# Kernel optimization log

Hardware: AMD Instinct MI355X
Metric: run time of the kernel (lower is better)

Reference implementation:

```python
import jax, jax.numpy as jnp
import numpy as np

DIM = 768
NUM_HEADS = 8
GROUPS = 2


def setup_inputs() -> dict:
    key = jax.random.key(0)
    ks = jax.random.split(key, 6)
    B, N, C = 8, 1024, DIM
    x = jax.random.normal(ks[0], (B, N, C), dtype=jnp.float32)
    # nn.Linear weights stored (out_features, in_features), applied as x @ W.T
    w_qkv = jax.random.normal(ks[1], (3 * C, C), dtype=jnp.float32) * 0.02
    g_dim = C // GROUPS
    w_g0 = jax.random.normal(ks[2], (3 * g_dim, g_dim), dtype=jnp.float32) * 0.02
    w_g1 = jax.random.normal(ks[3], (3 * g_dim, g_dim), dtype=jnp.float32) * 0.02
    w_proj = jax.random.normal(ks[4], (C, C), dtype=jnp.float32) * 0.02
    b_proj = jax.random.normal(ks[5], (C,), dtype=jnp.float32) * 0.02
    return {"x": x, "w_qkv": w_qkv, "w_g0": w_g0, "w_g1": w_g1,
            "w_proj": w_proj, "b_proj": b_proj}


def reference(x, w_qkv, w_g0, w_g1, w_proj, b_proj):
    B, N, C = x.shape
    H = NUM_HEADS
    hd = C // H
    scale = hd ** (-0.5)  # qk_scale=None -> head_dim^-0.5, reused in group attn
    g = GROUPS
    g_dim = C // g

    # ---- standard MHSA branch ----
    qkv = (x @ w_qkv.T).reshape(B, N, 3, H, hd)
    qkv = jnp.transpose(qkv, (2, 0, 3, 1, 4))  # (3, B, H, N, hd)
    q, k, v = qkv[0], qkv[1], qkv[2]
    attn = jax.nn.softmax(jnp.einsum('bhnd,bhmd->bhnm', q, k) * scale, axis=-1)
    origin = jnp.einsum('bhnm,bhmd->bhnd', attn, v)  # (B, H, N, hd)
    origin = origin.swapaxes(1, 2).reshape(B, N, g, g_dim)

    # ---- sequential per-group head-fusion branch ----
    xg = x.reshape(B, N, g, g_dim)
    head_x = jnp.zeros((B, N, g_dim), dtype=x.dtype)
    outputs = []
    for i, w in enumerate([w_g0, w_g1]):  # fixed small loop, g=2
        cur = xg[:, :, i] + head_x
        qkv2 = (cur @ w.T).reshape(B, N, 3, g_dim)
        q2, k2, v2 = qkv2[:, :, 0], qkv2[:, :, 1], qkv2[:, :, 2]
        a2 = jax.nn.softmax(jnp.einsum('bnd,bmd->bnm', q2, k2) * scale, axis=-1)
        head_x = jnp.einsum('bnm,bmd->bnd', a2, v2)
        outputs.append(head_x + origin[:, :, i])

    out = jnp.concatenate(outputs, axis=-1)
    return out @ w_proj.T + b_proj
```

## Files before the change

### kernel.cpp

```cpp
#include <hip/hip_runtime.h>
#include <cstdint>
#include <cstddef>

#define DEV_INLINE __device__ __forceinline__

typedef __bf16 bf16;
typedef __bf16 bf16x8 __attribute__((ext_vector_type(8)));
typedef float f32x4 __attribute__((ext_vector_type(4)));

static constexpr int Bb = 8;
static constexpr int Nn = 1024;
static constexpr int Cc = 768;
static constexpr int HD = 96;
static constexpr int GD = 384;
#define SCALE_ 0.1020620726159658f

DEV_INLINE void gload_lds16(void* lds, const void* g) {
  __builtin_amdgcn_global_load_lds(
      (__attribute__((address_space(1))) void*)(void*)g,
      (__attribute__((address_space(3))) void*)lds, 16, 0, 0);
}

__global__ void k_f32_to_bf16(const float* __restrict__ src, bf16* __restrict__ dst, int n) {
  int i = (blockIdx.x * 256 + threadIdx.x) * 8;
  if (i >= n) return;
  float4 a = *(const float4*)(src + i);
  float4 b = *(const float4*)(src + i + 4);
  bf16x8 o;
  o[0] = (bf16)a.x; o[1] = (bf16)a.y; o[2] = (bf16)a.z; o[3] = (bf16)a.w;
  o[4] = (bf16)b.x; o[5] = (bf16)b.y; o[6] = (bf16)b.z; o[7] = (bf16)b.w;
  *(bf16x8*)(dst + i) = o;
}

__global__ void k_make_cur(const float* __restrict__ x, const float* __restrict__ hx,
                           bf16* __restrict__ cur, int gi) {
  int t = blockIdx.x * 256 + threadIdx.x;
  int m = t / 48;
  int d0 = (t % 48) * 8;
  const float* xr = x + (size_t)m * Cc + gi * GD + d0;
  float4 a = *(const float4*)xr;
  float4 b = *(const float4*)(xr + 4);
  if (gi) {
    const float* hr = hx + (size_t)m * GD + d0;
    float4 c = *(const float4*)hr;
    float4 d = *(const float4*)(hr + 4);
    a.x += c.x; a.y += c.y; a.z += c.z; a.w += c.w;
    b.x += d.x; b.y += d.y; b.z += d.z; b.w += d.w;
  }
  bf16x8 o;
  o[0] = (bf16)a.x; o[1] = (bf16)a.y; o[2] = (bf16)a.z; o[3] = (bf16)a.w;
  o[4] = (bf16)b.x; o[5] = (bf16)b.y; o[6] = (bf16)b.z; o[7] = (bf16)b.w;
  *(bf16x8*)(cur + (size_t)m * GD + d0) = o;
}

template <int EPI>
__global__ __launch_bounds__(256, 2)
void k_gemm(const bf16* __restrict__ A, const bf16* __restrict__ W, int K,
            int aZ, int wZ,
            bf16* __restrict__ o0, bf16* __restrict__ o1, bf16* __restrict__ o2,
            float* __restrict__ f0, const float* __restrict__ bias,
            const float* __restrict__ origin, int gi) {
  const int bm = blockIdx.x, bn = blockIdx.y, bz = blockIdx.z;
  const int tid = threadIdx.x;
  const int wave = tid >> 6, lane = tid & 63;
  const int wr = wave >> 1, wc = wave & 1;
  const int l15 = lane & 15, l4 = lane >> 4;

  A += (size_t)bz * aZ;
  W += (size_t)bz * wZ;

  __shared__ bf16 As[128 * 32];
  __shared__ bf16 Bs[128 * 32];

  f32x4 acc[4][4] = {};

  const int t8 = tid * 8;
  const int r0 = t8 >> 5, c0 = t8 & 31;
  const int r1 = r0 + 64;
  const bf16* Arow0 = A + (size_t)(bm * 128 + r0) * K + c0;
  const bf16* Arow1 = A + (size_t)(bm * 128 + r1) * K + c0;
  const bf16* Brow0 = W + (size_t)(bn * 128 + r0) * K + c0;
  const bf16* Brow1 = W + (size_t)(bn * 128 + r1) * K + c0;
  bf16* sA0 = &As[wave * 512];
  bf16* sA1 = &As[2048 + wave * 512];
  bf16* sB0 = &Bs[wave * 512];
  bf16* sB1 = &Bs[2048 + wave * 512];

  for (int k0 = 0; k0 < K; k0 += 32) {
    gload_lds16(sA0, Arow0 + k0);
    gload_lds16(sA1, Arow1 + k0);
    gload_lds16(sB0, Brow0 + k0);
    gload_lds16(sB1, Brow1 + k0);
    __syncthreads();
    bf16x8 af[4], bfr[4];
#pragma unroll
    for (int i = 0; i < 4; ++i) {
      af[i]  = *(const bf16x8*)&As[(wr * 64 + i * 16 + l15) * 32 + l4 * 8];
      bfr[i] = *(const bf16x8*)&Bs[(wc * 64 + i * 16 + l15) * 32 + l4 * 8];
    }
#pragma unroll
    for (int i = 0; i < 4; ++i)
#pragma unroll
      for (int j = 0; j < 4; ++j)
        acc[i][j] = __builtin_amdgcn_mfma_f32_16x16x32_bf16(af[i], bfr[j], acc[i][j], 0, 0, 0);
    __syncthreads();
  }

#pragma unroll
  for (int i = 0; i < 4; ++i) {
    const int mbase = bm * 128 + wr * 64 + i * 16 + l4 * 4;
#pragma unroll
    for (int j = 0; j < 4; ++j) {
      const int col = bn * 128 + wc * 64 + j * 16 + l15;
#pragma unroll
      for (int r = 0; r < 4; ++r) {
        const int row = mbase + r;
        const float val = acc[i][j][r];
        if constexpr (EPI == 2) {
          f0[(size_t)row * 768 + col] = val + bias[col];
        } else if constexpr (EPI == 3) {
          o0[((size_t)bz * 1024 + row) * 1024 + col] = (bf16)(val * SCALE_);
        } else if constexpr (EPI == 4) {
          const size_t gr = (size_t)bz * 1024 + row;
          f0[gr * 384 + col] = val;
          const size_t ci = gr * 768 + gi * 384 + col;
          o1[ci] = (bf16)(val + origin[ci]);
        } else if constexpr (EPI == 0) {
          const int bb = row >> 10, n = row & 1023;
          const int sct = col / 768, rem = col % 768;
          const int hh = rem / 96, dd = rem % 96;
          const bf16 bv = (bf16)val;
          if (sct == 0)      o0[((size_t)(bb * 8 + hh) * 1024 + n) * 96 + dd] = bv;
          else if (sct == 1) o1[((size_t)(bb * 8 + hh) * 1024 + n) * 96 + dd] = bv;
          else               o2[((size_t)(bb * 8 + hh) * 96 + dd) * 1024 + n] = bv;
        } else {
          const int bb = row >> 10, n = row & 1023;
          const int sct = col / 384, dd = col % 384;
          const bf16 bv = (bf16)val;
          if (sct == 0)      o0[(size_t)row * 384 + dd] = bv;
          else if (sct == 1) o1[(size_t)row * 384 + dd] = bv;
          else               o2[((size_t)bb * 384 + dd) * 1024 + n] = bv;
        }
      }
    }
  }
}

__global__ __launch_bounds__(256)
void k_softmax_rows(bf16* __restrict__ SP) {
  const int row = blockIdx.x * 4 + (threadIdx.x >> 6);
  const int lane = threadIdx.x & 63;
  bf16* R = SP + (size_t)row * 1024 + lane * 16;
  bf16x8 a = *(const bf16x8*)R;
  bf16x8 b = *(const bf16x8*)(R + 8);
  float v[16];
#pragma unroll
  for (int i = 0; i < 8; ++i) { v[i] = (float)a[i]; v[8 + i] = (float)b[i]; }
  float mx = -1e30f;
#pragma unroll
  for (int i = 0; i < 16; ++i) mx = fmaxf(mx, v[i]);
  mx = fmaxf(mx, __shfl_xor(mx, 1));
  mx = fmaxf(mx, __shfl_xor(mx, 2));
  mx = fmaxf(mx, __shfl_xor(mx, 4));
  mx = fmaxf(mx, __shfl_xor(mx, 8));
  mx = fmaxf(mx, __shfl_xor(mx, 16));
  mx = fmaxf(mx, __shfl_xor(mx, 32));
  float s = 0.f;
#pragma unroll
  for (int i = 0; i < 16; ++i) { v[i] = __expf(v[i] - mx); s += v[i]; }
  s += __shfl_xor(s, 1);
  s += __shfl_xor(s, 2);
  s += __shfl_xor(s, 4);
  s += __shfl_xor(s, 8);
  s += __shfl_xor(s, 16);
  s += __shfl_xor(s, 32);
  const float inv = 1.f / s;
#pragma unroll
  for (int i = 0; i < 8; ++i) { a[i] = (bf16)(v[i] * inv); b[i] = (bf16)(v[8 + i] * inv); }
  *(bf16x8*)R = a;
  *(bf16x8*)(R + 8) = b;
}

__global__ __launch_bounds__(256, 2)
void k_flash_mha(const bf16* __restrict__ Q, const bf16* __restrict__ Kt,
                 const bf16* __restrict__ Vt, float* __restrict__ origin) {
  const int bh = blockIdx.x, qb = blockIdx.y;
  const int b = bh >> 3, h = bh & 7;
  const int wave = threadIdx.x >> 6, lane = threadIdx.x & 63;
  const int l15 = lane & 15, l4 = lane >> 4;
  const bf16* Qh = Q + (size_t)bh * Nn * HD;
  const bf16* Kh = Kt + (size_t)bh * Nn * HD;
  const bf16* Vh = Vt + (size_t)bh * HD * Nn;
  const int q0 = qb * 128 + wave * 32;

  bf16x8 qf[2][3];
#pragma unroll
  for (int mf = 0; mf < 2; ++mf)
#pragma unroll
    for (int kf = 0; kf < 3; ++kf)
      qf[mf][kf] = *(const bf16x8*)&Qh[(size_t)(q0 + mf * 16 + l15) * HD + kf * 32 + l4 * 8];

  f32x4 o[2][6] = {};
  float mrow[2][4], lrow[2][4];
#pragma unroll
  for (int mf = 0; mf < 2; ++mf)
#pragma unroll
    for (int r = 0; r < 4; ++r) { mrow[mf][r] = -1e30f; lrow[mf][r] = 0.f; }

  __shared__ bf16 Plds[4][32 * 88];
  bf16* Pl = &Plds[wave][0];

  for (int n0 = 0; n0 < Nn; n0 += 64) {
    f32x4 s[2][4] = {};
#pragma unroll
    for (int nf = 0; nf < 4; ++nf)
#pragma unroll
      for (int kf = 0; kf < 3; ++kf) {
        bf16x8 kfr = *(const bf16x8*)&Kh[(size_t)(n0 + nf * 16 + l15) * HD + kf * 32 + l4 * 8];
#pragma unroll
        for (int mf = 0; mf < 2; ++mf)
          s[mf][nf] = __builtin_amdgcn_mfma_f32_16x16x32_bf16(qf[mf][kf], kfr, s[mf][nf], 0, 0, 0);
      }
#pragma unroll
    for (int mf = 0; mf < 2; ++mf)
#pragma unroll
      for (int r = 0; r < 4; ++r) {
        float mx = -1e30f;
#pragma unroll
        for (int nf = 0; nf < 4; ++nf) {
          s[mf][nf][r] *= SCALE_;
          mx = fmaxf(mx, s[mf][nf][r]);
        }
        mx = fmaxf(mx, __shfl_xor(mx, 1));
        mx = fmaxf(mx, __shfl_xor(mx, 2));
        mx = fmaxf(mx, __shfl_xor(mx, 4));
        mx = fmaxf(mx, __shfl_xor(mx, 8));
        float mnew = fmaxf(mrow[mf][r], mx);
        float alpha = __expf(mrow[mf][r] - mnew);
        mrow[mf][r] = mnew;
        float ls = 0.f;
#pragma unroll
        for (int nf = 0; nf < 4; ++nf) {
          float p = __expf(s[mf][nf][r] - mnew);
          s[mf][nf][r] = p;
          ls += p;
        }
        ls += __shfl_xor(ls, 1); ls += __shfl_xor(ls, 2);
        ls += __shfl_xor(ls, 4); ls += __shfl_xor(ls, 8);
        lrow[mf][r] = lrow[mf][r] * alpha + ls;
#pragma unroll
        for (int df = 0; df < 6; ++df) o[mf][df][r] *= alpha;
      }
#pragma unroll
    for (int mf = 0; mf < 2; ++mf)
#pragma unroll
      for (int nf = 0; nf < 4; ++nf)
#pragma unroll
        for (int r = 0; r < 4; ++r)
          Pl[(mf * 16 + l4 * 4 + r) * 88 + nf * 16 + l15] = (bf16)s[mf][nf][r];
    bf16x8 pa[2][2];
#pragma unroll
    for (int mf = 0; mf < 2; ++mf)
#pragma unroll
      for (int kf2 = 0; kf2 < 2; ++kf2)
        pa[mf][kf2] = *(const bf16x8*)&Pl[(mf * 16 + l15) * 88 + kf2 * 32 + l4 * 8];
#pragma unroll
    for (int df = 0; df < 6; ++df)
#pragma unroll
      for (int kf2 = 0; kf2 < 2; ++kf2) {
        bf16x8 vf = *(const bf16x8*)&Vh[(size_t)(df * 16 + l15) * Nn + n0 + kf2 * 32 + l4 * 8];
#pragma unroll
        for (int mf = 0; mf < 2; ++mf)
          o[mf][df] = __builtin_amdgcn_mfma_f32_16x16x32_bf16(pa[mf][kf2], vf, o[mf][df], 0, 0, 0);
      }
  }

  float* Og = origin + (size_t)b * Nn * Cc + h * HD;
#pragma unroll
  for (int mf = 0; mf < 2; ++mf)
#pragma unroll
    for (int r = 0; r < 4; ++r) {
      const int row = q0 + mf * 16 + l4 * 4 + r;
      const float inv = 1.f / lrow[mf][r];
#pragma unroll
      for (int df = 0; df < 6; ++df)
        Og[(size_t)row * Cc + df * 16 + l15] = o[mf][df][r] * inv;
    }
}

extern "C" void kernel_launch(void* const* d_in, const int* in_sizes, int n_in,
                              void* d_out, int out_size, void* d_ws, size_t ws_size,
                              hipStream_t stream) {
  const float* x      = (const float*)d_in[0];
  const float* w_qkv  = (const float*)d_in[1];
  const float* w_g0   = (const float*)d_in[2];
  const float* w_g1   = (const float*)d_in[3];
  const float* w_proj = (const float*)d_in[4];
  const float* b_proj = (const float*)d_in[5];
  float* out = (float*)d_out;

  char* ws = (char*)d_ws;
  size_t off = 0;
  auto alloc = [&](size_t bytes) {
    char* p = ws + off;
    off += (bytes + 255) & ~(size_t)255;
    return p;
  };
  bf16* xb     = (bf16*)alloc((size_t)8192 * 768 * 2);
  bf16* wqkvb  = (bf16*)alloc((size_t)2304 * 768 * 2);
  bf16* wg0b   = (bf16*)alloc((size_t)1152 * 384 * 2);
  bf16* wg1b   = (bf16*)alloc((size_t)1152 * 384 * 2);
  bf16* wprojb = (bf16*)alloc((size_t)768 * 768 * 2);
  float* origin = (float*)alloc((size_t)8192 * 768 * 4);
  char* R = alloc((size_t)67108864);
  bf16* Qb = (bf16*)R;
  bf16* Kb = (bf16*)(R + 12582912);
  bf16* Vt = (bf16*)(R + 25165824);
  bf16* curb = (bf16*)R;
  bf16* q2   = (bf16*)(R + 6291456);
  bf16* k2   = (bf16*)(R + 12582912);
  bf16* v2t  = (bf16*)(R + 18874368);
  float* hx  = (float*)(R + 25165824);
  bf16* cat  = (bf16*)(R + 37748736);
  bf16* SP   = (bf16*)(R + 50331648);

  k_f32_to_bf16<<<dim3(3072), 256, 0, stream>>>(x, xb, 8192 * 768);
  k_f32_to_bf16<<<dim3(864), 256, 0, stream>>>(w_qkv, wqkvb, 2304 * 768);
  k_f32_to_bf16<<<dim3(216), 256, 0, stream>>>(w_g0, wg0b, 1152 * 384);
  k_f32_to_bf16<<<dim3(216), 256, 0, stream>>>(w_g1, wg1b, 1152 * 384);
  k_f32_to_bf16<<<dim3(288), 256, 0, stream>>>(w_proj, wprojb, 768 * 768);

  k_gemm<0><<<dim3(64, 18), 256, 0, stream>>>(xb, wqkvb, 768, 0, 0, Qb, Kb, Vt, nullptr, nullptr, nullptr, 0);
  k_flash_mha<<<dim3(64, 8), 256, 0, stream>>>(Qb, Kb, Vt, origin);

  for (int gi = 0; gi < 2; ++gi) {
    const bf16* wg = gi ? wg1b : wg0b;
    k_make_cur<<<dim3(1536), 256, 0, stream>>>(x, hx, curb, gi);
    k_gemm<1><<<dim3(64, 9), 256, 0, stream>>>(curb, wg, 384, 0, 0, q2, k2, v2t, nullptr, nullptr, nullptr, 0);
    k_gemm<3><<<dim3(8, 8, 8), 256, 0, stream>>>(q2, k2, 384, 1024 * 384, 1024 * 384,
                                                 SP, nullptr, nullptr, nullptr, nullptr, nullptr, 0);
    k_softmax_rows<<<dim3(2048), 256, 0, stream>>>(SP);
    k_gemm<4><<<dim3(8, 3, 8), 256, 0, stream>>>(SP, v2t, 1024, 1024 * 1024, 384 * 1024,
                                                 nullptr, cat, nullptr, hx, nullptr, origin, gi);
  }

  k_gemm<2><<<dim3(64, 6), 256, 0, stream>>>(cat, wprojb, 768, 0, 0, nullptr, nullptr, nullptr, out, b_proj, nullptr, 0);
}
```

Before: 448.8 us.

## Fuse input conversions, shrink flash tiles, add lazy softmax rescaling

Five f32-to-bf16 conversion launches are merged into one kernel that picks its source and destination by index range, removing launch overhead. The flash MHA kernel now gives each wave 16 query rows instead of 32, doubling the grid and raising launch bounds to 4 blocks per SM for more occupancy. Online softmax rescaling is skipped unless some row's running max grows by more than 8, cutting exp and multiply work. The trade-off is that K and V fragments are reused across fewer query rows, so global loads per MFMA double.

Result: no change. 453.5 us (+1.1%).

```diff
diff --git a/kernel.cpp b/kernel.cpp
--- a/kernel.cpp
+++ b/kernel.cpp
@@ -21,15 +21,25 @@
       (__attribute__((address_space(3))) void*)lds, 16, 0, 0);
 }
 
-__global__ void k_f32_to_bf16(const float* __restrict__ src, bf16* __restrict__ dst, int n) {
-  int i = (blockIdx.x * 256 + threadIdx.x) * 8;
-  if (i >= n) return;
-  float4 a = *(const float4*)(src + i);
-  float4 b = *(const float4*)(src + i + 4);
+__global__ void k_convert_all(const float* __restrict__ x, const float* __restrict__ wqkv,
+                              const float* __restrict__ wg0, const float* __restrict__ wg1,
+                              const float* __restrict__ wproj,
+                              bf16* __restrict__ xb, bf16* __restrict__ wqkvb,
+                              bf16* __restrict__ wg0b, bf16* __restrict__ wg1b,
+                              bf16* __restrict__ wprojb) {
+  const int i = (blockIdx.x * 256 + threadIdx.x) * 8;
+  const float* src; bf16* dst; int off;
+  if (i < 6291456)      { src = x;     dst = xb;     off = i; }
+  else if (i < 8060928) { src = wqkv;  dst = wqkvb;  off = i - 6291456; }
+  else if (i < 8503296) { src = wg0;   dst = wg0b;   off = i - 8060928; }
+  else if (i < 8945664) { src = wg1;   dst = wg1b;   off = i - 8503296; }
+  else                  { src = wproj; dst = wprojb; off = i - 8945664; }
+  float4 a = *(const float4*)(src + off);
+  float4 b = *(const float4*)(src + off + 4);
   bf16x8 o;
   o[0] = (bf16)a.x; o[1] = (bf16)a.y; o[2] = (bf16)a.z; o[3] = (bf16)a.w;
   o[4] = (bf16)b.x; o[5] = (bf16)b.y; o[6] = (bf16)b.z; o[7] = (bf16)b.w;
-  *(bf16x8*)(dst + i) = o;
+  *(bf16x8*)(dst + off) = o;
 }
 
 __global__ void k_make_cur(const float* __restrict__ x, const float* __restrict__ hx,
@@ -181,7 +191,7 @@
   *(bf16x8*)(R + 8) = b;
 }
 
-__global__ __launch_bounds__(256, 2)
+__global__ __launch_bounds__(256, 4)
 void k_flash_mha(const bf16* __restrict__ Q, const bf16* __restrict__ Kt,
                  const bf16* __restrict__ Vt, float* __restrict__ origin) {
   const int bh = blockIdx.x, qb = blockIdx.y;
@@ -191,101 +201,99 @@
   const bf16* Qh = Q + (size_t)bh * Nn * HD;
   const bf16* Kh = Kt + (size_t)bh * Nn * HD;
   const bf16* Vh = Vt + (size_t)bh * HD * Nn;
-  const int q0 = qb * 128 + wave * 32;
-
-  bf16x8 qf[2][3];
-#pragma unroll
-  for (int mf = 0; mf < 2; ++mf)
-#pragma unroll
-    for (int kf = 0; kf < 3; ++kf)
-      qf[mf][kf] = *(const bf16x8*)&Qh[(size_t)(q0 + mf * 16 + l15) * HD + kf * 32 + l4 * 8];
-
-  f32x4 o[2][6] = {};
-  float mrow[2][4], lrow[2][4];
-#pragma unroll
-  for (int mf = 0; mf < 2; ++mf)
-#pragma unroll
-    for (int r = 0; r < 4; ++r) { mrow[mf][r] = -1e30f; lrow[mf][r] = 0.f; }
-
-  __shared__ bf16 Plds[4][32 * 88];
+  const int q0 = qb * 64 + wave * 16;
+
+  bf16x8 qf[3];
+#pragma unroll
+  for (int kf = 0; kf < 3; ++kf)
+    qf[kf] = *(const bf16x8*)&Qh[(size_t)(q0 + l15) * HD + kf * 32 + l4 * 8];
+
+  f32x4 o[6] = {};
+  float mrow[4], lrow[4];
+#pragma unroll
+  for (int r = 0; r < 4; ++r) { mrow[r] = -1e30f; lrow[r] = 0.f; }
+
+  __shared__ bf16 Plds[4][16 * 88];
   bf16* Pl = &Plds[wave][0];
 
   for (int n0 = 0; n0 < Nn; n0 += 64) {
-    f32x4 s[2][4] = {};
+    f32x4 s[4] = {};
 #pragma unroll
     for (int nf = 0; nf < 4; ++nf)
 #pragma unroll
       for (int kf = 0; kf < 3; ++kf) {
         bf16x8 kfr = *(const bf16x8*)&Kh[(size_t)(n0 + nf * 16 + l15) * HD + kf * 32 + l4 * 8];
-#pragma unroll
-        for (int mf = 0; mf < 2; ++mf)
-          s[mf][nf] = __builtin_amdgcn_mfma_f32_16x16x32_bf16(qf[mf][kf], kfr, s[mf][nf], 0, 0, 0);
-      }
-#pragma unroll
-    for (int mf = 0; mf < 2; ++mf)
+        s[nf] = __builtin_amdgcn_mfma_f32_16x16x32_bf16(qf[kf], kfr, s[nf], 0, 0, 0);
+      }
+    float pmax[4];
+#pragma unroll
+    for (int r = 0; r < 4; ++r) {
+      float mx = -1e30f;
+#pragma unroll
+      for (int nf = 0; nf < 4; ++nf) {
+        s[nf][r] *= SCALE_;
+        mx = fmaxf(mx, s[nf][r]);
+      }
+      mx = fmaxf(mx, __shfl_xor(mx, 1));
+      mx = fmaxf(mx, __shfl_xor(mx, 2));
+      mx = fmaxf(mx, __shfl_xor(mx, 4));
+      mx = fmaxf(mx, __shfl_xor(mx, 8));
+      pmax[r] = mx;
+    }
+    bool need = false;
+#pragma unroll
+    for (int r = 0; r < 4; ++r) need = need || (pmax[r] > mrow[r] + 8.f);
+    if (__any(need)) {
 #pragma unroll
       for (int r = 0; r < 4; ++r) {
-        float mx = -1e30f;
-#pragma unroll
-        for (int nf = 0; nf < 4; ++nf) {
-          s[mf][nf][r] *= SCALE_;
-          mx = fmaxf(mx, s[mf][nf][r]);
-        }
-        mx = fmaxf(mx, __shfl_xor(mx, 1));
-        mx = fmaxf(mx, __shfl_xor(mx, 2));
-        mx = fmaxf(mx, __shfl_xor(mx, 4));
-        mx = fmaxf(mx, __shfl_xor(mx, 8));
-        float mnew = fmaxf(mrow[mf][r], mx);
-        float alpha = __expf(mrow[mf][r] - mnew);
-        mrow[mf][r] = mnew;
-        float ls = 0.f;
-#pragma unroll
-        for (int nf = 0; nf < 4; ++nf) {
-          float p = __expf(s[mf][nf][r] - mnew);
-          s[mf][nf][r] = p;
-          ls += p;
-        }
-        ls += __shfl_xor(ls, 1); ls += __shfl_xor(ls, 2);
-        ls += __shfl_xor(ls, 4); ls += __shfl_xor(ls, 8);
-        lrow[mf][r] = lrow[mf][r] * alpha + ls;
-#pragma unroll
-        for (int df = 0; df < 6; ++df) o[mf][df][r] *= alpha;
-      }
-#pragma unroll
-    for (int mf = 0; mf < 2; ++mf)
-#pragma unroll
-      for (int nf = 0; nf < 4; ++nf)
-#pragma unroll
-        for (int r = 0; r < 4; ++r)
-          Pl[(mf * 16 + l4 * 4 + r) * 88 + nf * 16 + l15] = (bf16)s[mf][nf][r];
-    bf16x8 pa[2][2];
-#pragma unroll
-    for (int mf = 0; mf < 2; ++mf)
-#pragma unroll
-      for (int kf2 = 0; kf2 < 2; ++kf2)
-        pa[mf][kf2] = *(const bf16x8*)&Pl[(mf * 16 + l15) * 88 + kf2 * 32 + l4 * 8];
+        const float mnew = fmaxf(mrow[r], pmax[r]);
+        const float alpha = __expf(mrow[r] - mnew);
+        mrow[r] = mnew;
+        lrow[r] *= alpha;
+#pragma unroll
+        for (int df = 0; df < 6; ++df) o[df][r] *= alpha;
+      }
+    }
+#pragma unroll
+    for (int r = 0; r < 4; ++r) {
+      float ls = 0.f;
+#pragma unroll
+      for (int nf = 0; nf < 4; ++nf) {
+        const float p = __expf(s[nf][r] - mrow[r]);
+        s[nf][r] = p;
+        ls += p;
+      }
+      ls += __shfl_xor(ls, 1); ls += __shfl_xor(ls, 2);
+      ls += __shfl_xor(ls, 4); ls += __shfl_xor(ls, 8);
+      lrow[r] += ls;
+    }
+#pragma unroll
+    for (int nf = 0; nf < 4; ++nf)
+#pragma unroll
+      for (int r = 0; r < 4; ++r)
+        Pl[(l4 * 4 + r) * 88 + nf * 16 + l15] = (bf16)s[nf][r];
+    bf16x8 pa[2];
+#pragma unroll
+    for (int kf2 = 0; kf2 < 2; ++kf2)
+      pa[kf2] = *(const bf16x8*)&Pl[l15 * 88 + kf2 * 32 + l4 * 8];
 #pragma unroll
     for (int df = 0; df < 6; ++df)
 #pragma unroll
       for (int kf2 = 0; kf2 < 2; ++kf2) {
         bf16x8 vf = *(const bf16x8*)&Vh[(size_t)(df * 16 + l15) * Nn + n0 + kf2 * 32 + l4 * 8];
-#pragma unroll
-        for (int mf = 0; mf < 2; ++mf)
-          o[mf][df] = __builtin_amdgcn_mfma_f32_16x16x32_bf16(pa[mf][kf2], vf, o[mf][df], 0, 0, 0);
+        o[df] = __builtin_amdgcn_mfma_f32_16x16x32_bf16(pa[kf2], vf, o[df], 0, 0, 0);
       }
   }
 
   float* Og = origin + (size_t)b * Nn * Cc + h * HD;
 #pragma unroll
-  for (int mf = 0; mf < 2; ++mf)
-#pragma unroll
-    for (int r = 0; r < 4; ++r) {
-      const int row = q0 + mf * 16 + l4 * 4 + r;
-      const float inv = 1.f / lrow[mf][r];
-#pragma unroll
-      for (int df = 0; df < 6; ++df)
-        Og[(size_t)row * Cc + df * 16 + l15] = o[mf][df][r] * inv;
-    }
+  for (int r = 0; r < 4; ++r) {
+    const int row = q0 + l4 * 4 + r;
+    const float inv = 1.f / lrow[r];
+#pragma unroll
+    for (int df = 0; df < 6; ++df)
+      Og[(size_t)row * Cc + df * 16 + l15] = o[df][r] * inv;
+  }
 }
 
 extern "C" void kernel_launch(void* const* d_in, const int* in_sizes, int n_in,
@@ -324,14 +332,11 @@
   bf16* cat  = (bf16*)(R + 37748736);
   bf16* SP   = (bf16*)(R + 50331648);
 
-  k_f32_to_bf16<<<dim3(3072), 256, 0, stream>>>(x, xb, 8192 * 768);
-  k_f32_to_bf16<<<dim3(864), 256, 0, stream>>>(w_qkv, wqkvb, 2304 * 768);
-  k_f32_to_bf16<<<dim3(216), 256, 0, stream>>>(w_g0, wg0b, 1152 * 384);
-  k_f32_to_bf16<<<dim3(216), 256, 0, stream>>>(w_g1, wg1b, 1152 * 384);
-  k_f32_to_bf16<<<dim3(288), 256, 0, stream>>>(w_proj, wprojb, 768 * 768);
+  k_convert_all<<<dim3(4656), 256, 0, stream>>>(x, w_qkv, w_g0, w_g1, w_proj,
+                                                xb, wqkvb, wg0b, wg1b, wprojb);
 
   k_gemm<0><<<dim3(64, 18), 256, 0, stream>>>(xb, wqkvb, 768, 0, 0, Qb, Kb, Vt, nullptr, nullptr, nullptr, 0);
-  k_flash_mha<<<dim3(64, 8), 256, 0, stream>>>(Qb, Kb, Vt, origin);
+  k_flash_mha<<<dim3(64, 16), 256, 0, stream>>>(Qb, Kb, Vt, origin);
 
   for (int gi = 0; gi < 2; ++gi) {
     const bf16* wg = gi ? wg1b : wg0b;
```
